# Kernel optimization log

Hardware: AMD Instinct MI355X
Metric: run time of the kernel (lower is better)

The kernel has to match this reference:

```python
import jax, jax.numpy as jnp
import numpy as np

EPS = 1e-7  # K.epsilon()

def squash(v, axis=-1):
    s2 = jnp.sum(jnp.square(v), axis=axis, keepdims=True)
    scale = s2 / (1.0 + s2) / jnp.sqrt(s2 + EPS)
    return scale * v

def setup_inputs() -> dict:
    key = jax.random.key(0)
    k1, k2 = jax.random.split(key)
    B, I, J, K, M = 32, 64, 1152, 32, 16
    inputs = jax.random.normal(k1, (B, J, M), dtype=jnp.float32)
    # glorot_uniform-scaled init for W [num_capsule, input_num_capsule, dim_capsule, input_dim_capsule]
    limit = np.sqrt(6.0 / (M + K))
    W = jax.random.uniform(k2, (I, J, K, M), dtype=jnp.float32, minval=-limit, maxval=limit)
    return {"inputs": inputs, "W": W}

def reference(inputs, W):
    routings = 3
    # u_hat: [B, I, J, K]
    u_hat = jnp.einsum('ijkm,bjm->bijk', W, inputs)
    B, I, J, _ = u_hat.shape
    b = jnp.zeros((B, I, J), dtype=u_hat.dtype)
    outputs = None
    for i in range(routings):
        c = jax.nn.softmax(b, axis=1)                    # softmax over output capsules
        s = jnp.einsum('bij,bijk->bik', c, u_hat)        # weighted sum over input capsules
        outputs = squash(s)
        if i < routings - 1:
            agreement = jnp.einsum('bik,bijk->bij', outputs, u_hat)
            b = b + agreement
    return outputs
```

## Files before the change

### kernel.cpp

```cpp
#include <hip/hip_runtime.h>


#define Ii 64
#define Jj 1152
#define Kk 32
#define Bb 32
#define NJB2 72

typedef short  bf16x8 __attribute__((ext_vector_type(8)));
typedef float  f32x16 __attribute__((ext_vector_type(16)));
typedef float  f32x4  __attribute__((ext_vector_type(4)));

__device__ __forceinline__ void split2(float a, float b, unsigned &hi, unsigned &lo){
  unsigned ua = __float_as_uint(a), ub = __float_as_uint(b);
  unsigned ha = ua & 0xFFFF0000u, hb = ub & 0xFFFF0000u;
  hi = (ha >> 16) | hb;
  float la = a - __uint_as_float(ha);
  float lb = b - __uint_as_float(hb);
  lo = ((__float_as_uint(la) & 0xFFFF0000u) >> 16) | (__float_as_uint(lb) & 0xFFFF0000u);
}

__device__ __forceinline__ void split8(const float* v, bf16x8 &hi, bf16x8 &lo){
  union U { bf16x8 v; unsigned u[4]; } H, L;
#pragma unroll
  for (int p=0;p<4;p++) split2(v[2*p], v[2*p+1], H.u[p], L.u[p]);
  hi = H.v; lo = L.v;
}

__device__ __forceinline__ ushort f2bf_rne(float f){
  unsigned u = __float_as_uint(f);
  return (ushort)((u + 0x7FFFu + ((u >> 16) & 1u)) >> 16);
}

#define MFMA(A,B,C) __builtin_amdgcn_mfma_f32_32x32x16_bf16(A,B,C,0,0,0)

template<int FIRST>
__global__ __launch_bounds__(256, 2)
void k_s(const float* __restrict__ Wp, const ushort* __restrict__ Wbi,
         ushort* __restrict__ Wbo, const float* __restrict__ xp,
         const float* __restrict__ brt, const float* __restrict__ zp,
         ushort* __restrict__ spart)
{
  __shared__ float red[4*1088];
  const int t  = threadIdx.x;
  const int w  = t >> 6, lane = t & 63;
  const int kk = lane & 31;
  const int h  = lane >> 5;
  const int b  = lane & 31;
  const int i0 = blockIdx.y * 4;
  const int j0 = blockIdx.x * 16 + w * 4;

  bf16x8 Bh[4], Bl[4];
  float zi[4];
#pragma unroll
  for (int jj=0;jj<4;jj++){
    const int j = j0 + jj;
    float x8[8];
    *(f32x4*)(x8)   = *(const f32x4*)(xp + (b*Jj + j)*16 + h*8);
    *(f32x4*)(x8+4) = *(const f32x4*)(xp + (b*Jj + j)*16 + h*8 + 4);
    split8(x8, Bh[jj], Bl[jj]);
    if (!FIRST) zi[jj] = 1.0f / zp[j*32 + b];
  }

  f32x16 acc[4];
#pragma unroll
  for (int ii=0;ii<4;ii++) acc[ii] = {};

#pragma unroll
  for (int ii=0; ii<4; ++ii){
    const int i = i0 + ii;
#pragma unroll
    for (int jj=0;jj<4;jj++){
      const size_t eoff = (size_t)(i*Jj + j0+jj)*512 + kk*16 + h*8;
      f32x16 d = {};
      if (FIRST){
        float w8[8];
        *(f32x4*)(w8)   = *(const f32x4*)(Wp + eoff);
        *(f32x4*)(w8+4) = *(const f32x4*)(Wp + eoff + 4);
        bf16x8 Ah, Al;
        split8(w8, Ah, Al);
        *reinterpret_cast<bf16x8*>(Wbo + eoff) = Ah;
        d = MFMA(Ah, Bh[jj], d);
        d = MFMA(Ah, Bl[jj], d);
        d = MFMA(Al, Bh[jj], d);
      } else {
        const bf16x8 Ah = *reinterpret_cast<const bf16x8*>(Wbi + eoff);
        d = MFMA(Ah, Bh[jj], d);
        d = MFMA(Ah, Bl[jj], d);
      }
      float cw;
      if (FIRST) cw = 0.015625f;
      else {
        const float bv = brt[(i*Jj + j0+jj)*32 + b];
        cw = __expf(bv) * zi[jj];
      }
#pragma unroll
      for (int r=0;r<16;r++) acc[ii][r] += cw * d[r];
    }
  }

#pragma unroll
  for (int ii=0; ii<4; ++ii){
    __syncthreads();
#pragma unroll
    for (int r=0;r<16;r++) red[w*1088 + lane*17 + r] = acc[ii][r];
    __syncthreads();
    ushort4 outv;
    {
      float sx, sy, sz, sw;
#pragma unroll
      for (int q=0;q<4;q++){
        const int v  = t*4 + q;
        const int lv = v >> 4, r = v & 15;
        float sum = 0.f;
#pragma unroll
        for (int ww=0;ww<4;ww++) sum += red[ww*1088 + lv*17 + r];
        if (q==0) sx=sum; else if (q==1) sy=sum; else if (q==2) sz=sum; else sw=sum;
      }
      outv.x = f2bf_rne(sx); outv.y = f2bf_rne(sy);
      outv.z = f2bf_rne(sz); outv.w = f2bf_rne(sw);
    }
    *(ushort4*)&spart[((size_t)blockIdx.x*Ii + (i0+ii))*1024 + t*4] = outv;
  }
}

template<int TR>
__global__ __launch_bounds__(256)
void k_redsq(const ushort* __restrict__ spart, float* __restrict__ outp)
{
  const int i = blockIdx.x, t = threadIdx.x;
  float a0=0.f, a1=0.f, a2=0.f, a3=0.f;
#pragma unroll 8
  for (int jb=0;jb<NJB2;jb++){
    const ushort4 u = *(const ushort4*)&spart[((size_t)jb*Ii + i)*1024 + t*4];
    a0 += __uint_as_float((unsigned)u.x << 16);
    a1 += __uint_as_float((unsigned)u.y << 16);
    a2 += __uint_as_float((unsigned)u.z << 16);
    a3 += __uint_as_float((unsigned)u.w << 16);
  }

  const int b2 = (t>>2)&31, hh = t>>7, t3 = t&3;
  float ss = a0*a0 + a1*a1 + a2*a2 + a3*a3;
  ss += __shfl_xor(ss,1);
  ss += __shfl_xor(ss,2);
  __shared__ float sp2[2][32];
  if (t3 == 0) sp2[hh][b2] = ss;
  __syncthreads();
  const float s2 = sp2[0][b2] + sp2[1][b2];
  const float scale = s2/(1.f+s2) * rsqrtf(s2 + 1e-7f);
  const float vals[4] = {a0*scale, a1*scale, a2*scale, a3*scale};
#pragma unroll
  for (int q=0;q<4;q++){
    const int kcap = q + 8*t3 + 4*hh;
    if (TR) outp[(i*Kk + kcap)*Bb + b2] = vals[q];
    else    outp[((size_t)b2*Ii + i)*Kk + kcap] = vals[q];
  }
}

template<int ADD>
__global__ __launch_bounds__(256, 2)
void k_ag(const ushort* __restrict__ Wb, const float* __restrict__ xp,
          const float* __restrict__ ot, float* __restrict__ brt,
          float* __restrict__ zp)
{
  const int t  = threadIdx.x;
  const int w  = t >> 6, lane = t & 63;
  const int kk = lane & 31;
  const int h  = lane >> 5;
  const int b  = lane & 31;
  const int i0 = blockIdx.y * 4;
  const int j0 = blockIdx.x * 16 + w * 4;

  bf16x8 Bh[4], Bl[4];
#pragma unroll
  for (int jj=0;jj<4;jj++){
    const int j = j0 + jj;
    float x8[8];
    *(f32x4*)(x8)   = *(const f32x4*)(xp + (b*Jj + j)*16 + h*8);
    *(f32x4*)(x8+4) = *(const f32x4*)(xp + (b*Jj + j)*16 + h*8 + 4);
    split8(x8, Bh[jj], Bl[jj]);
  }

  float ez[4] = {0.f, 0.f, 0.f, 0.f};

#pragma unroll
  for (int ii=0; ii<4; ++ii){
    const int i = i0 + ii;
    float ov[16];
#pragma unroll
    for (int r=0;r<16;r++){
      const int kcap = (r & 3) + 8*(r >> 2) + 4*h;
      ov[r] = ot[(i*Kk + kcap)*Bb + b];
    }
#pragma unroll
    for (int jj=0;jj<4;jj++){
      const size_t eoff = (size_t)(i*Jj + j0+jj)*512 + kk*16 + h*8;
      const bf16x8 Ah = *reinterpret_cast<const bf16x8*>(Wb + eoff);
      f32x16 d = {};
      d = MFMA(Ah, Bh[jj], d);
      d = MFMA(Ah, Bl[jj], d);
      float ap = 0.f;
#pragma unroll
      for (int r=0;r<16;r++) ap += ov[r]*d[r];
      ap += __shfl_xor(ap, 32);
      if (h == 0){
        const int idx = (i*Jj + j0+jj)*32 + b;
        const float prev = ADD ? brt[idx] : 0.f;
        const float bn = prev + ap;
        brt[idx] = bn;
        ez[jj] += __expf(bn);
      }
    }
  }
  if (h == 0){
#pragma unroll
    for (int jj=0;jj<4;jj++)
      atomicAdd(&zp[(j0+jj)*32 + b], ez[jj]);
  }
}

extern "C" void kernel_launch(void* const* d_in, const int* in_sizes, int n_in,
                              void* d_out, int out_size, void* d_ws, size_t ws_size,
                              hipStream_t stream)
{
  const float* x  = (const float*)d_in[0];
  const float* Wp = (const float*)d_in[1];
  float* out = (float*)d_out;
  float* ws  = (float*)d_ws;
  ushort* spart = (ushort*)ws;
  float* br    = ws + 2359296;
  float* z     = ws + 4718592;
  float* ot    = ws + 4755456;
  ushort* Wbf  = (ushort*)(ws + 4820992);

  dim3 gs(NJB2, 16), bs(256);

  k_s<1><<<gs, bs, 0, stream>>>(Wp, nullptr, Wbf, x, nullptr, nullptr, spart);
  k_redsq<1><<<dim3(64), bs, 0, stream>>>(spart, ot);
  hipMemsetAsync(z, 0, 36864*sizeof(float), stream);
  k_ag<0><<<gs, bs, 0, stream>>>(Wbf, x, ot, br, z);

  k_s<0><<<gs, bs, 0, stream>>>(nullptr, Wbf, nullptr, x, br, z, spart);
  k_redsq<1><<<dim3(64), bs, 0, stream>>>(spart, ot);
  hipMemsetAsync(z, 0, 36864*sizeof(float), stream);
  k_ag<1><<<gs, bs, 0, stream>>>(Wbf, x, ot, br, z);

  k_s<0><<<gs, bs, 0, stream>>>(nullptr, Wbf, nullptr, x, br, z, spart);
  k_redsq<0><<<dim3(64), bs, 0, stream>>>(spart, out);
}
```

Before: 136.3 us.

## Halve per-block i-tile in later passes and fold z zeroing into reduce

The non-first scoring kernel and the agreement kernel now process two output capsules per block instead of four, doubling grid size and raising the occupancy hint to 4 blocks per SM. The separate memset of the softmax denominator buffer is removed, and that zeroing is folded into the reduce/squash kernel. This cuts launch count and adds parallelism, but it doubles the redundant x loads and splits per block, and tightens the register budget.

```diff
diff --git a/kernel.cpp b/kernel.cpp
--- a/kernel.cpp
+++ b/kernel.cpp
@@ -35,19 +35,20 @@
 #define MFMA(A,B,C) __builtin_amdgcn_mfma_f32_32x32x16_bf16(A,B,C,0,0,0)
 
 template<int FIRST>
-__global__ __launch_bounds__(256, 2)
+__global__ __launch_bounds__(256, FIRST ? 2 : 4)
 void k_s(const float* __restrict__ Wp, const ushort* __restrict__ Wbi,
          ushort* __restrict__ Wbo, const float* __restrict__ xp,
          const float* __restrict__ brt, const float* __restrict__ zp,
          ushort* __restrict__ spart)
 {
+  constexpr int IT = FIRST ? 4 : 2;
   __shared__ float red[4*1088];
   const int t  = threadIdx.x;
   const int w  = t >> 6, lane = t & 63;
   const int kk = lane & 31;
   const int h  = lane >> 5;
   const int b  = lane & 31;
-  const int i0 = blockIdx.y * 4;
+  const int i0 = blockIdx.y * IT;
   const int j0 = blockIdx.x * 16 + w * 4;
 
   bf16x8 Bh[4], Bl[4];
@@ -62,12 +63,12 @@
     if (!FIRST) zi[jj] = 1.0f / zp[j*32 + b];
   }
 
-  f32x16 acc[4];
-#pragma unroll
-  for (int ii=0;ii<4;ii++) acc[ii] = {};
-
-#pragma unroll
-  for (int ii=0; ii<4; ++ii){
+  f32x16 acc[IT];
+#pragma unroll
+  for (int ii=0;ii<IT;ii++) acc[ii] = {};
+
+#pragma unroll
+  for (int ii=0; ii<IT; ++ii){
     const int i = i0 + ii;
 #pragma unroll
     for (int jj=0;jj<4;jj++){
@@ -100,14 +101,14 @@
   }
 
 #pragma unroll
-  for (int ii=0; ii<4; ++ii){
+  for (int ii=0; ii<IT; ++ii){
     __syncthreads();
 #pragma unroll
     for (int r=0;r<16;r++) red[w*1088 + lane*17 + r] = acc[ii][r];
     __syncthreads();
     ushort4 outv;
     {
-      float sx, sy, sz, sw;
+      float s0=0.f, s1=0.f, s2v=0.f, s3=0.f;
 #pragma unroll
       for (int q=0;q<4;q++){
         const int v  = t*4 + q;
@@ -115,20 +116,27 @@
         float sum = 0.f;
 #pragma unroll
         for (int ww=0;ww<4;ww++) sum += red[ww*1088 + lv*17 + r];
-        if (q==0) sx=sum; else if (q==1) sy=sum; else if (q==2) sz=sum; else sw=sum;
-      }
-      outv.x = f2bf_rne(sx); outv.y = f2bf_rne(sy);
-      outv.z = f2bf_rne(sz); outv.w = f2bf_rne(sw);
+        if (q==0) s0=sum; else if (q==1) s1=sum; else if (q==2) s2v=sum; else s3=sum;
+      }
+      outv.x = f2bf_rne(s0); outv.y = f2bf_rne(s1);
+      outv.z = f2bf_rne(s2v); outv.w = f2bf_rne(s3);
     }
     *(ushort4*)&spart[((size_t)blockIdx.x*Ii + (i0+ii))*1024 + t*4] = outv;
   }
 }
 
-template<int TR>
+template<int TR, int ZZ>
 __global__ __launch_bounds__(256)
-void k_redsq(const ushort* __restrict__ spart, float* __restrict__ outp)
+void k_redsq(const ushort* __restrict__ spart, float* __restrict__ outp,
+             float* __restrict__ zp)
 {
   const int i = blockIdx.x, t = threadIdx.x;
+  if (ZZ){
+    const int base = blockIdx.x * 576;
+    zp[base + t] = 0.f;
+    zp[base + 256 + t] = 0.f;
+    if (t < 64) zp[base + 512 + t] = 0.f;
+  }
   float a0=0.f, a1=0.f, a2=0.f, a3=0.f;
 #pragma unroll 8
   for (int jb=0;jb<NJB2;jb++){
@@ -158,7 +166,7 @@
 }
 
 template<int ADD>
-__global__ __launch_bounds__(256, 2)
+__global__ __launch_bounds__(256, 4)
 void k_ag(const ushort* __restrict__ Wb, const float* __restrict__ xp,
           const float* __restrict__ ot, float* __restrict__ brt,
           float* __restrict__ zp)
@@ -168,7 +176,7 @@
   const int kk = lane & 31;
   const int h  = lane >> 5;
   const int b  = lane & 31;
-  const int i0 = blockIdx.y * 4;
+  const int i0 = blockIdx.y * 2;
   const int j0 = blockIdx.x * 16 + w * 4;
 
   bf16x8 Bh[4], Bl[4];
@@ -184,7 +192,7 @@
   float ez[4] = {0.f, 0.f, 0.f, 0.f};
 
 #pragma unroll
-  for (int ii=0; ii<4; ++ii){
+  for (int ii=0; ii<2; ++ii){
     const int i = i0 + ii;
     float ov[16];
 #pragma unroll
@@ -233,18 +241,16 @@
   float* ot    = ws + 4755456;
   ushort* Wbf  = (ushort*)(ws + 4820992);
 
-  dim3 gs(NJB2, 16), bs(256);
-
-  k_s<1><<<gs, bs, 0, stream>>>(Wp, nullptr, Wbf, x, nullptr, nullptr, spart);
-  k_redsq<1><<<dim3(64), bs, 0, stream>>>(spart, ot);
-  hipMemsetAsync(z, 0, 36864*sizeof(float), stream);
-  k_ag<0><<<gs, bs, 0, stream>>>(Wbf, x, ot, br, z);
-
-  k_s<0><<<gs, bs, 0, stream>>>(nullptr, Wbf, nullptr, x, br, z, spart);
-  k_redsq<1><<<dim3(64), bs, 0, stream>>>(spart, ot);
-  hipMemsetAsync(z, 0, 36864*sizeof(float), stream);
-  k_ag<1><<<gs, bs, 0, stream>>>(Wbf, x, ot, br, z);
-
-  k_s<0><<<gs, bs, 0, stream>>>(nullptr, Wbf, nullptr, x, br, z, spart);
-  k_redsq<0><<<dim3(64), bs, 0, stream>>>(spart, out);
-}
+  dim3 gs1(NJB2, 16), gs2(NJB2, 32), bs(256);
+
+  k_s<1><<<gs1, bs, 0, stream>>>(Wp, nullptr, Wbf, x, nullptr, nullptr, spart);
+  k_redsq<1,1><<<dim3(64), bs, 0, stream>>>(spart, ot, z);
+  k_ag<0><<<gs2, bs, 0, stream>>>(Wbf, x, ot, br, z);
+
+  k_s<0><<<gs2, bs, 0, stream>>>(nullptr, Wbf, nullptr, x, br, z, spart);
+  k_redsq<1,1><<<dim3(64), bs, 0, stream>>>(spart, ot, z);
+  k_ag<1><<<gs2, bs, 0, stream>>>(Wbf, x, ot, br, z);
+
+  k_s<0><<<gs2, bs, 0, stream>>>(nullptr, Wbf, nullptr, x, br, z, spart);
+  k_redsq<0,0><<<dim3(64), bs, 0, stream>>>(spart, out, nullptr);
+}
```

Result: slower. 141.4 us (+3.7%).
